# Kernel optimization log

Measured on AMD Instinct MI355X. Metric: run time of the kernel, lower is better.

Reference implementation:

```python
import jax, jax.numpy as jnp
import numpy as np

H = 128      # num_hidden
NIN = 384    # num_in
FF = 4 * H   # feedforward dim
SCALE = 30.0
EPS = 1e-5


def _linear(x, w, b):
    # torch Linear: weight [out, in]
    return x @ w.T + b


def _ln(x, g, b):
    mu = jnp.mean(x, axis=-1, keepdims=True)
    var = jnp.var(x, axis=-1, keepdims=True)
    return (x - mu) * jax.lax.rsqrt(var + EPS) * g + b


def setup_inputs() -> dict:
    key = jax.random.key(0)
    ks = jax.random.split(key, 16)
    B, N, K = 2, 2048, 48
    s = 0.05
    return {
        "h_V": jax.random.normal(ks[0], (B, N, H), jnp.float32),
        "h_E": jax.random.normal(ks[1], (B, N, K, NIN), jnp.float32),
        "mask_V": jnp.ones((B, N), jnp.float32),
        "mask_attend": jnp.ones((B, N, K), jnp.float32),
        "W1_w": jax.random.normal(ks[2], (H, H + NIN), jnp.float32) * s,
        "W1_b": jnp.zeros((H,), jnp.float32),
        "W2_w": jax.random.normal(ks[3], (H, H), jnp.float32) * s,
        "W2_b": jnp.zeros((H,), jnp.float32),
        "W3_w": jax.random.normal(ks[4], (H, H), jnp.float32) * s,
        "W3_b": jnp.zeros((H,), jnp.float32),
        "ln1_g": jnp.ones((H,), jnp.float32),
        "ln1_b": jnp.zeros((H,), jnp.float32),
        "ln2_g": jnp.ones((H,), jnp.float32),
        "ln2_b": jnp.zeros((H,), jnp.float32),
        "Win_w": jax.random.normal(ks[5], (FF, H), jnp.float32) * s,
        "Win_b": jnp.zeros((FF,), jnp.float32),
        "Wout_w": jax.random.normal(ks[6], (H, FF), jnp.float32) * s,
        "Wout_b": jnp.zeros((H,), jnp.float32),
    }


def reference(h_V, h_E, mask_V, mask_attend,
              W1_w, W1_b, W2_w, W2_b, W3_w, W3_b,
              ln1_g, ln1_b, ln2_g, ln2_b,
              Win_w, Win_b, Wout_w, Wout_b):
    gelu = lambda x: jax.nn.gelu(x, approximate=False)  # torch GELU (erf)
    B, N, K, _ = h_E.shape
    # expand-concat: [B,N,K,H+NIN]
    h_V_expand = jnp.broadcast_to(h_V[:, :, None, :], (B, N, K, H))
    h_EV = jnp.concatenate([h_V_expand, h_E], axis=-1)
    # 3-layer message MLP
    h_message = _linear(gelu(_linear(gelu(_linear(h_EV, W1_w, W1_b)), W2_w, W2_b)), W3_w, W3_b)
    h_message = mask_attend[..., None] * h_message
    dh = jnp.sum(h_message, axis=-2) / SCALE
    h = _ln(h_V + dh, ln1_g, ln1_b)  # dropout = identity (eval)
    dh = _linear(gelu(_linear(h, Win_w, Win_b)), Wout_w, Wout_b)
    h = _ln(h + dh, ln2_g, ln2_b)
    return mask_V[..., None] * h
```

## Files before the change

### kernel.cpp

```cpp
#include <hip/hip_runtime.h>
#include <math.h>


typedef __bf16 bf16;
typedef __attribute__((ext_vector_type(8))) __bf16 bf16x8;
typedef __attribute__((ext_vector_type(4))) float f32x4;
typedef __attribute__((ext_vector_type(4))) unsigned uint4v;

__device__ __forceinline__ unsigned pk2bf(float a, float b) {
    unsigned ua = __builtin_bit_cast(unsigned, a) + 0x8000u;
    unsigned ub = __builtin_bit_cast(unsigned, b) + 0x8000u;
    return __builtin_amdgcn_perm(ub, ua, 0x07060302u);
}
__device__ __forceinline__ bf16 f2bf(float f) {
    unsigned short s = (unsigned short)((__builtin_bit_cast(unsigned, f) + 0x8000u) >> 16);
    return __builtin_bit_cast(bf16, s);
}
__device__ __forceinline__ bf16x8 pack8(float4 v0, float4 v1) {
    uint4v p;
    p.x = pk2bf(v0.x, v0.y); p.y = pk2bf(v0.z, v0.w);
    p.z = pk2bf(v1.x, v1.y); p.w = pk2bf(v1.z, v1.w);
    return __builtin_bit_cast(bf16x8, p);
}
__device__ __forceinline__ float gelu_f(float x) {
    float u = 1.595769122f * x * fmaf(0.044715f, x * x, 1.0f);
    float e = __expf(-u);
    return x * __builtin_amdgcn_rcpf(1.0f + e);
}
__device__ __forceinline__ f32x4 mfma16(bf16x8 a, bf16x8 b, f32x4 c) {
    return __builtin_amdgcn_mfma_f32_16x16x32_bf16(a, b, c, 0, 0, 0);
}

#define WS_W2   65536
#define WS_W3   81920
#define WS_WIN  98304
#define WS_WOUT 163840
#define WS_TOTAL_W 229376
#define WS_H1_BYTES 458752

__global__ void convert_weights(const float* __restrict__ W1, const float* __restrict__ W2,
                                const float* __restrict__ W3, const float* __restrict__ Win,
                                const float* __restrict__ Wout, bf16* __restrict__ ws) {
    int i = blockIdx.x * 256 + threadIdx.x;
    if (i < WS_W2)              ws[i] = f2bf(W1[i]);
    else if (i < WS_W3)         ws[i] = f2bf(W2[i - WS_W2]);
    else if (i < WS_WIN)        ws[i] = f2bf(W3[i - WS_W3]);
    else if (i < WS_WOUT)       ws[i] = f2bf(Win[i - WS_WIN]);
    else if (i < WS_TOTAL_W)    ws[i] = f2bf(Wout[i - WS_WOUT]);
}

__global__ __launch_bounds__(256, 4)
void msg_kernel(const float* __restrict__ h_V, const float* __restrict__ h_E,
                const float* __restrict__ mask_attend,
                const bf16* __restrict__ W1b, const bf16* __restrict__ W2b,
                const bf16* __restrict__ W3b,
                const float* __restrict__ b1, const float* __restrict__ b2,
                const float* __restrict__ b3,
                const float* __restrict__ ln1g, const float* __restrict__ ln1b,
                float* __restrict__ h1out) {
    __shared__ __align__(16) bf16 m1[48 * 136];
    __shared__ __align__(16) bf16 m2[48 * 136];
    __shared__ float tbuf[128];

    const int tid  = threadIdx.x;
    const int wave = tid >> 6;
    const int lane = tid & 63;
    const int q    = lane >> 4;
    const int c15  = lane & 15;
    const int g    = blockIdx.x;
    const int n0c  = wave * 32 + c15;

    const f32x4 zero = {0.f, 0.f, 0.f, 0.f};

    f32x4 acc0[2] = {zero, zero};
    {
        const float* pV  = h_V + (size_t)g * 128 + q * 8;
        const bf16* pWv0 = W1b + (size_t)n0c * 512 + q * 8;
        const bf16* pWv1 = pWv0 + 16 * 512;
#pragma unroll
        for (int s = 0; s < 4; ++s) {
            float4 v0 = *(const float4*)(pV + s * 32);
            float4 v1 = *(const float4*)(pV + s * 32 + 4);
            bf16x8 af = pack8(v0, v1);
            bf16x8 w0 = *(const bf16x8*)(pWv0 + s * 32);
            bf16x8 w1 = *(const bf16x8*)(pWv1 + s * 32);
            acc0[0] = mfma16(af, w0, acc0[0]);
            acc0[1] = mfma16(af, w1, acc0[1]);
        }
    }

    f32x4 acc[3][2];
#pragma unroll
    for (int mt = 0; mt < 3; ++mt) { acc[mt][0] = zero; acc[mt][1] = zero; }
    {
        const float* pE0 = h_E + ((size_t)g * 48 + c15) * 384 + q * 8;
        const float* pE1 = pE0 + 16 * 384;
        const float* pE2 = pE1 + 16 * 384;
        const bf16* pW0 = W1b + (size_t)n0c * 512 + 128 + q * 8;
        const bf16* pW1 = pW0 + 16 * 512;
#pragma unroll
        for (int ks = 0; ks < 12; ++ks) {
            bf16x8 w0 = *(const bf16x8*)(pW0 + ks * 32);
            bf16x8 w1 = *(const bf16x8*)(pW1 + ks * 32);
            float4 a00 = *(const float4*)(pE0 + ks * 32);
            float4 a01 = *(const float4*)(pE0 + ks * 32 + 4);
            float4 a10 = *(const float4*)(pE1 + ks * 32);
            float4 a11 = *(const float4*)(pE1 + ks * 32 + 4);
            float4 a20 = *(const float4*)(pE2 + ks * 32);
            float4 a21 = *(const float4*)(pE2 + ks * 32 + 4);
            bf16x8 f0 = pack8(a00, a01);
            bf16x8 f1 = pack8(a10, a11);
            bf16x8 f2 = pack8(a20, a21);
            acc[0][0] = mfma16(f0, w0, acc[0][0]);
            acc[0][1] = mfma16(f0, w1, acc[0][1]);
            acc[1][0] = mfma16(f1, w0, acc[1][0]);
            acc[1][1] = mfma16(f1, w1, acc[1][1]);
            acc[2][0] = mfma16(f2, w0, acc[2][0]);
            acc[2][1] = mfma16(f2, w1, acc[2][1]);
        }
    }
    {
        const float bb0 = b1[n0c], bb1 = b1[n0c + 16];
#pragma unroll
        for (int mt = 0; mt < 3; ++mt)
#pragma unroll
            for (int r = 0; r < 4; ++r) {
                const int row = mt * 16 + q * 4 + r;
                m1[row * 136 + n0c]      = f2bf(gelu_f(acc[mt][0][r] + acc0[0][r] + bb0));
                m1[row * 136 + n0c + 16] = f2bf(gelu_f(acc[mt][1][r] + acc0[1][r] + bb1));
            }
    }
    __syncthreads();

    f32x4 acc2[3][2];
#pragma unroll
    for (int mt = 0; mt < 3; ++mt) { acc2[mt][0] = zero; acc2[mt][1] = zero; }
    {
        bf16x8 w[4][2];
        const bf16* pW20 = W2b + (size_t)n0c * 128 + q * 8;
        const bf16* pW21 = pW20 + 16 * 128;
#pragma unroll
        for (int s = 0; s < 4; ++s) {
            w[s][0] = *(const bf16x8*)(pW20 + s * 32);
            w[s][1] = *(const bf16x8*)(pW21 + s * 32);
        }
        const bf16* pA = m1 + c15 * 136 + q * 8;
#pragma unroll
        for (int s = 0; s < 4; ++s)
#pragma unroll
            for (int mt = 0; mt < 3; ++mt) {
                bf16x8 af = *(const bf16x8*)(pA + mt * 16 * 136 + s * 32);
                acc2[mt][0] = mfma16(af, w[s][0], acc2[mt][0]);
                acc2[mt][1] = mfma16(af, w[s][1], acc2[mt][1]);
            }
    }
    {
        const float bb0 = b2[n0c], bb1 = b2[n0c + 16];
#pragma unroll
        for (int mt = 0; mt < 3; ++mt)
#pragma unroll
            for (int r = 0; r < 4; ++r) {
                const int row = mt * 16 + q * 4 + r;
                m2[row * 136 + n0c]      = f2bf(gelu_f(acc2[mt][0][r] + bb0));
                m2[row * 136 + n0c + 16] = f2bf(gelu_f(acc2[mt][1][r] + bb1));
            }
    }
    __syncthreads();

    f32x4 acc3[3][2];
#pragma unroll
    for (int mt = 0; mt < 3; ++mt) { acc3[mt][0] = zero; acc3[mt][1] = zero; }
    {
        bf16x8 w[4][2];
        const bf16* pW30 = W3b + (size_t)n0c * 128 + q * 8;
        const bf16* pW31 = pW30 + 16 * 128;
#pragma unroll
        for (int s = 0; s < 4; ++s) {
            w[s][0] = *(const bf16x8*)(pW30 + s * 32);
            w[s][1] = *(const bf16x8*)(pW31 + s * 32);
        }
        const bf16* pA = m2 + c15 * 136 + q * 8;
#pragma unroll
        for (int s = 0; s < 4; ++s)
#pragma unroll
            for (int mt = 0; mt < 3; ++mt) {
                bf16x8 af = *(const bf16x8*)(pA + mt * 16 * 136 + s * 32);
                acc3[mt][0] = mfma16(af, w[s][0], acc3[mt][0]);
                acc3[mt][1] = mfma16(af, w[s][1], acc3[mt][1]);
            }
    }
    {
        const float bb0 = b3[n0c], bb1 = b3[n0c + 16];
        float s0 = 0.f, s1 = 0.f;
#pragma unroll
        for (int mt = 0; mt < 3; ++mt)
#pragma unroll
            for (int r = 0; r < 4; ++r) {
                const int row = mt * 16 + q * 4 + r;
                const float mv = mask_attend[(size_t)g * 48 + row];
                s0 += (acc3[mt][0][r] + bb0) * mv;
                s1 += (acc3[mt][1][r] + bb1) * mv;
            }
        s0 += __shfl_xor(s0, 16); s0 += __shfl_xor(s0, 32);
        s1 += __shfl_xor(s1, 16); s1 += __shfl_xor(s1, 32);
        if (lane < 16) {
            tbuf[n0c]      = h_V[(size_t)g * 128 + n0c]      + s0 * (1.0f / 30.0f);
            tbuf[n0c + 16] = h_V[(size_t)g * 128 + n0c + 16] + s1 * (1.0f / 30.0f);
        }
    }
    __syncthreads();

    if (wave == 0) {
        const float x0 = tbuf[lane];
        const float x1 = tbuf[lane + 64];
        float sm = x0 + x1, sq = x0 * x0 + x1 * x1;
#pragma unroll
        for (int off = 1; off < 64; off <<= 1) { sm += __shfl_xor(sm, off); sq += __shfl_xor(sq, off); }
        const float mu  = sm * (1.0f / 128.0f);
        const float var = sq * (1.0f / 128.0f) - mu * mu;
        const float inv = rsqrtf(var + 1e-5f);
        h1out[(size_t)g * 128 + lane]      = (x0 - mu) * inv * ln1g[lane]      + ln1b[lane];
        h1out[(size_t)g * 128 + 64 + lane] = (x1 - mu) * inv * ln1g[64 + lane] + ln1b[64 + lane];
    }
}

__global__ __launch_bounds__(512, 4)
void ffn_kernel(const float* __restrict__ h1, const bf16* __restrict__ Winb,
                const bf16* __restrict__ Woutb,
                const float* __restrict__ bin, const float* __restrict__ bout,
                const float* __restrict__ ln2g, const float* __restrict__ ln2b,
                const float* __restrict__ mask_V, float* __restrict__ out) {
    __shared__ __align__(16) bf16 a2[16 * 136];
    __shared__ __align__(16) bf16 ff[16 * 520];
    __shared__ float tb0[16 * 132];
    __shared__ float tb1[16 * 132];

    const int tid  = threadIdx.x;
    const int wave = tid >> 6;
    const int lane = tid & 63;
    const int q    = lane >> 4;
    const int c15  = lane & 15;
    const int r0g  = blockIdx.x * 8;
    const f32x4 zero = {0.f, 0.f, 0.f, 0.f};

    {
        const int row = tid >> 5;
        const int c4  = tid & 31;
        const int gr  = min(r0g + row, 4095);
        float4 v = *(const float4*)(h1 + (size_t)gr * 128 + c4 * 4);
        uint2 pk; pk.x = pk2bf(v.x, v.y); pk.y = pk2bf(v.z, v.w);
        *(uint2*)(a2 + row * 136 + c4 * 4) = pk;
    }
    __syncthreads();

    {
        f32x4 accA[4] = {zero, zero, zero, zero};
        const bf16* pA = a2 + c15 * 136 + q * 8;
#pragma unroll
        for (int s = 0; s < 4; ++s) {
            bf16x8 af = *(const bf16x8*)(pA + s * 32);
#pragma unroll
            for (int nt = 0; nt < 4; ++nt) {
                const int n = wave * 64 + nt * 16 + c15;
                bf16x8 wb = *(const bf16x8*)(Winb + (size_t)n * 128 + s * 32 + q * 8);
                accA[nt] = mfma16(af, wb, accA[nt]);
            }
        }
#pragma unroll
        for (int nt = 0; nt < 4; ++nt) {
            const int col = wave * 64 + nt * 16 + c15;
            const float bb = bin[col];
#pragma unroll
            for (int r = 0; r < 4; ++r)
                ff[(q * 4 + r) * 520 + col] = f2bf(gelu_f(accA[nt][r] + bb));
        }
    }
    __syncthreads();

    {
        const int kh = wave & 1, nq = wave >> 1;
        f32x4 accB[2] = {zero, zero};
        const bf16* pF = ff + c15 * 520 + kh * 256 + q * 8;
#pragma unroll
        for (int s = 0; s < 8; ++s) {
            bf16x8 af = *(const bf16x8*)(pF + s * 32);
#pragma unroll
            for (int nt = 0; nt < 2; ++nt) {
                const int n = nq * 32 + nt * 16 + c15;
                bf16x8 wb = *(const bf16x8*)(Woutb + (size_t)n * 512 + kh * 256 + s * 32 + q * 8);
                accB[nt] = mfma16(af, wb, accB[nt]);
            }
        }
        float* tb = kh ? tb1 : tb0;
#pragma unroll
        for (int nt = 0; nt < 2; ++nt) {
            const int col = nq * 32 + nt * 16 + c15;
#pragma unroll
            for (int r = 0; r < 4; ++r) {
                const int row = q * 4 + r;
                float v = accB[nt][r];
                if (kh == 0) {
                    const int gr = min(r0g + row, 4095);
                    v += bout[col] + h1[(size_t)gr * 128 + col];
                }
                tb[row * 132 + col] = v;
            }
        }
    }
    __syncthreads();

    {
        const int row = wave;
        const int gr  = r0g + row;
        const float x0 = tb0[row * 132 + lane]      + tb1[row * 132 + lane];
        const float x1 = tb0[row * 132 + 64 + lane] + tb1[row * 132 + 64 + lane];
        float sm = x0 + x1, sq = x0 * x0 + x1 * x1;
#pragma unroll
        for (int off = 1; off < 64; off <<= 1) { sm += __shfl_xor(sm, off); sq += __shfl_xor(sq, off); }
        const float mu  = sm * (1.0f / 128.0f);
        const float var = sq * (1.0f / 128.0f) - mu * mu;
        const float inv = rsqrtf(var + 1e-5f);
        const float mv  = mask_V[gr];
        out[(size_t)gr * 128 + lane]      = mv * ((x0 - mu) * inv * ln2g[lane]      + ln2b[lane]);
        out[(size_t)gr * 128 + 64 + lane] = mv * ((x1 - mu) * inv * ln2g[64 + lane] + ln2b[64 + lane]);
    }
}

extern "C" void kernel_launch(void* const* d_in, const int* in_sizes, int n_in,
                              void* d_out, int out_size, void* d_ws, size_t ws_size,
                              hipStream_t stream) {
    const float* h_V         = (const float*)d_in[0];
    const float* h_E         = (const float*)d_in[1];
    const float* mask_V      = (const float*)d_in[2];
    const float* mask_attend = (const float*)d_in[3];
    const float* W1w  = (const float*)d_in[4];
    const float* W1bb = (const float*)d_in[5];
    const float* W2w  = (const float*)d_in[6];
    const float* W2bb = (const float*)d_in[7];
    const float* W3w  = (const float*)d_in[8];
    const float* W3bb = (const float*)d_in[9];
    const float* ln1g = (const float*)d_in[10];
    const float* ln1b = (const float*)d_in[11];
    const float* ln2g = (const float*)d_in[12];
    const float* ln2b = (const float*)d_in[13];
    const float* Winw  = (const float*)d_in[14];
    const float* Winbb = (const float*)d_in[15];
    const float* Woutw  = (const float*)d_in[16];
    const float* Woutbb = (const float*)d_in[17];

    bf16* wsb   = (bf16*)d_ws;
    bf16* W1c   = wsb;
    bf16* W2c   = wsb + WS_W2;
    bf16* W3c   = wsb + WS_W3;
    bf16* Winc  = wsb + WS_WIN;
    bf16* Woutc = wsb + WS_WOUT;
    float* h1   = (float*)((char*)d_ws + WS_H1_BYTES);

    convert_weights<<<896, 256, 0, stream>>>(W1w, W2w, W3w, Winw, Woutw, wsb);
    msg_kernel<<<4096, 256, 0, stream>>>(h_V, h_E, mask_attend, W1c, W2c, W3c,
                                         W1bb, W2bb, W3bb, ln1g, ln1b, h1);
    ffn_kernel<<<512, 512, 0, stream>>>(h1, Winc, Woutc, Winbb, Woutbb,
                                        ln2g, ln2b, mask_V, (float*)d_out);
}
```

Measured before the change: 608.0 us.

## Pre-convert h_E to bf16 and DMA edge tiles into swizzled LDS

A new pass converts h_E to bf16 in the workspace. A new message kernel then loads each node's 48x384 edge tile straight into LDS with global_load_lds, using an XOR swizzle, and issues the h_V part of the W1 product while that load is in flight. This is meant to replace many scattered fp32 global loads and in-register packing with asynchronous bulk copies. The cost is an extra full read and write of h_E, plus a dependence on workspace size, with the old kernel kept as a fallback. The FFN kernel is also reshaped to 16 rows per 256-thread block with no K-split, which removes the second partial-sum buffer.

Result: faster. 570.6 us (-6.1%).

```diff
diff --git a/kernel.cpp b/kernel.cpp
--- a/kernel.cpp
+++ b/kernel.cpp
@@ -30,13 +30,19 @@
 __device__ __forceinline__ f32x4 mfma16(bf16x8 a, bf16x8 b, f32x4 c) {
     return __builtin_amdgcn_mfma_f32_16x16x32_bf16(a, b, c, 0, 0, 0);
 }
+__device__ __forceinline__ void dma16(const void* g, void* l) {
+    __builtin_amdgcn_global_load_lds(
+        (const __attribute__((address_space(1))) unsigned int*)g,
+        (__attribute__((address_space(3))) unsigned int*)l, 16, 0, 0);
+}
 
 #define WS_W2   65536
 #define WS_W3   81920
 #define WS_WIN  98304
 #define WS_WOUT 163840
 #define WS_TOTAL_W 229376
-#define WS_H1_BYTES 458752
+#define WS_H1_OFF  458752
+#define WS_HEB_OFF 2555904ull
 
 __global__ void convert_weights(const float* __restrict__ W1, const float* __restrict__ W2,
                                 const float* __restrict__ W3, const float* __restrict__ Win,
@@ -47,6 +53,200 @@
     else if (i < WS_WIN)        ws[i] = f2bf(W3[i - WS_W3]);
     else if (i < WS_WOUT)       ws[i] = f2bf(Win[i - WS_WIN]);
     else if (i < WS_TOTAL_W)    ws[i] = f2bf(Wout[i - WS_WOUT]);
+}
+
+__global__ void convert_hE(const float* __restrict__ he, bf16* __restrict__ out, long long n) {
+    size_t i = ((size_t)blockIdx.x * 256 + threadIdx.x) * 8;
+    if ((long long)i + 8 > n) return;
+    float4 v0 = *(const float4*)(he + i);
+    float4 v1 = *(const float4*)(he + i + 4);
+    *(bf16x8*)(out + i) = pack8(v0, v1);
+}
+
+__global__ __launch_bounds__(256, 3)
+void msg_kernel_b(const float* __restrict__ h_V, const bf16* __restrict__ hEb,
+                  const float* __restrict__ mask_attend,
+                  const bf16* __restrict__ W1b, const bf16* __restrict__ W2b,
+                  const bf16* __restrict__ W3b,
+                  const float* __restrict__ b1, const float* __restrict__ b2,
+                  const float* __restrict__ b3,
+                  const float* __restrict__ ln1g, const float* __restrict__ ln1b,
+                  float* __restrict__ h1out) {
+    __shared__ __align__(16) char smem[50432];
+    bf16*  Ab   = (bf16*)smem;
+    bf16*  m2   = (bf16*)smem;
+    bf16*  m1   = (bf16*)(smem + 36864);
+    float* tbuf = (float*)(smem + 49920);
+
+    const int tid  = threadIdx.x;
+    const int wave = tid >> 6;
+    const int lane = tid & 63;
+    const int q    = lane >> 4;
+    const int c15  = lane & 15;
+    const int g    = blockIdx.x;
+    const int n0c  = wave * 32 + c15;
+    const f32x4 zero = {0.f, 0.f, 0.f, 0.f};
+
+    float4 pv0[4], pv1[4];
+    bf16x8 pw0[4], pw1[4];
+    {
+        const float* pV  = h_V + (size_t)g * 128 + q * 8;
+        const bf16* pWv0 = W1b + (size_t)n0c * 512 + q * 8;
+        const bf16* pWv1 = pWv0 + 16 * 512;
+#pragma unroll
+        for (int s = 0; s < 4; ++s) {
+            pv0[s] = *(const float4*)(pV + s * 32);
+            pv1[s] = *(const float4*)(pV + s * 32 + 4);
+            pw0[s] = *(const bf16x8*)(pWv0 + s * 32);
+            pw1[s] = *(const bf16x8*)(pWv1 + s * 32);
+        }
+    }
+
+    {
+        const bf16* eb = hEb + (size_t)g * 48 * 384;
+#pragma unroll
+        for (int i = 0; i < 9; ++i) {
+            const int off = wave * 9216 + i * 1024 + lane * 16;
+            const int x   = off >> 8;
+            const int row = (x * 21846) >> 16;
+            const int seg = (off - row * 768) >> 4;
+            const int ss  = (seg & 48) | ((seg & 15) ^ (row & 15));
+            dma16(eb + row * 384 + ss * 8, smem + wave * 9216 + i * 1024);
+        }
+    }
+
+    f32x4 acc0[2] = {zero, zero};
+#pragma unroll
+    for (int s = 0; s < 4; ++s) {
+        bf16x8 af = pack8(pv0[s], pv1[s]);
+        acc0[0] = mfma16(af, pw0[s], acc0[0]);
+        acc0[1] = mfma16(af, pw1[s], acc0[1]);
+    }
+    __syncthreads();
+
+    f32x4 acc[3][2];
+#pragma unroll
+    for (int mt = 0; mt < 3; ++mt) { acc[mt][0] = zero; acc[mt][1] = zero; }
+    {
+        const bf16* pW0 = W1b + (size_t)n0c * 512 + 128 + q * 8;
+        const bf16* pW1 = pW0 + 16 * 512;
+#pragma unroll
+        for (int s = 0; s < 12; ++s) {
+            bf16x8 w0 = *(const bf16x8*)(pW0 + s * 32);
+            bf16x8 w1 = *(const bf16x8*)(pW1 + s * 32);
+            const int sq = s * 4 + q;
+            const int p  = (sq & 48) | ((sq & 15) ^ c15);
+#pragma unroll
+            for (int mt = 0; mt < 3; ++mt) {
+                bf16x8 af = *(const bf16x8*)(Ab + (mt * 16 + c15) * 384 + p * 8);
+                acc[mt][0] = mfma16(af, w0, acc[mt][0]);
+                acc[mt][1] = mfma16(af, w1, acc[mt][1]);
+            }
+        }
+    }
+    {
+        const float bb0 = b1[n0c], bb1 = b1[n0c + 16];
+#pragma unroll
+        for (int mt = 0; mt < 3; ++mt)
+#pragma unroll
+            for (int r = 0; r < 4; ++r) {
+                const int row = mt * 16 + q * 4 + r;
+                m1[row * 136 + n0c]      = f2bf(gelu_f(acc[mt][0][r] + acc0[0][r] + bb0));
+                m1[row * 136 + n0c + 16] = f2bf(gelu_f(acc[mt][1][r] + acc0[1][r] + bb1));
+            }
+    }
+    __syncthreads();
+
+    f32x4 acc2[3][2];
+#pragma unroll
+    for (int mt = 0; mt < 3; ++mt) { acc2[mt][0] = zero; acc2[mt][1] = zero; }
+    {
+        bf16x8 w[4][2];
+        const bf16* pW20 = W2b + (size_t)n0c * 128 + q * 8;
+        const bf16* pW21 = pW20 + 16 * 128;
+#pragma unroll
+        for (int s = 0; s < 4; ++s) {
+            w[s][0] = *(const bf16x8*)(pW20 + s * 32);
+            w[s][1] = *(const bf16x8*)(pW21 + s * 32);
+        }
+        const bf16* pA = m1 + c15 * 136 + q * 8;
+#pragma unroll
+        for (int s = 0; s < 4; ++s)
+#pragma unroll
+            for (int mt = 0; mt < 3; ++mt) {
+                bf16x8 af = *(const bf16x8*)(pA + mt * 16 * 136 + s * 32);
+                acc2[mt][0] = mfma16(af, w[s][0], acc2[mt][0]);
+                acc2[mt][1] = mfma16(af, w[s][1], acc2[mt][1]);
+            }
+    }
+    {
+        const float bb0 = b2[n0c], bb1 = b2[n0c + 16];
+#pragma unroll
+        for (int mt = 0; mt < 3; ++mt)
+#pragma unroll
+            for (int r = 0; r < 4; ++r) {
+                const int row = mt * 16 + q * 4 + r;
+                m2[row * 136 + n0c]      = f2bf(gelu_f(acc2[mt][0][r] + bb0));
+                m2[row * 136 + n0c + 16] = f2bf(gelu_f(acc2[mt][1][r] + bb1));
+            }
+    }
+    __syncthreads();
+
+    f32x4 acc3[3][2];
+#pragma unroll
+    for (int mt = 0; mt < 3; ++mt) { acc3[mt][0] = zero; acc3[mt][1] = zero; }
+    {
+        bf16x8 w[4][2];
+        const bf16* pW30 = W3b + (size_t)n0c * 128 + q * 8;
+        const bf16* pW31 = pW30 + 16 * 128;
+#pragma unroll
+        for (int s = 0; s < 4; ++s) {
+            w[s][0] = *(const bf16x8*)(pW30 + s * 32);
+            w[s][1] = *(const bf16x8*)(pW31 + s * 32);
+        }
+        const bf16* pA = m2 + c15 * 136 + q * 8;
+#pragma unroll
+        for (int s = 0; s < 4; ++s)
+#pragma unroll
+            for (int mt = 0; mt < 3; ++mt) {
+                bf16x8 af = *(const bf16x8*)(pA + mt * 16 * 136 + s * 32);
+                acc3[mt][0] = mfma16(af, w[s][0], acc3[mt][0]);
+                acc3[mt][1] = mfma16(af, w[s][1], acc3[mt][1]);
+            }
+    }
+    {
+        const float bb0 = b3[n0c], bb1 = b3[n0c + 16];
+        float s0 = 0.f, s1 = 0.f;
+#pragma unroll
+        for (int mt = 0; mt < 3; ++mt)
+#pragma unroll
+            for (int r = 0; r < 4; ++r) {
+                const int row = mt * 16 + q * 4 + r;
+                const float mv = mask_attend[(size_t)g * 48 + row];
+                s0 += (acc3[mt][0][r] + bb0) * mv;
+                s1 += (acc3[mt][1][r] + bb1) * mv;
+            }
+        s0 += __shfl_xor(s0, 16); s0 += __shfl_xor(s0, 32);
+        s1 += __shfl_xor(s1, 16); s1 += __shfl_xor(s1, 32);
+        if (lane < 16) {
+            tbuf[n0c]      = h_V[(size_t)g * 128 + n0c]      + s0 * (1.0f / 30.0f);
+            tbuf[n0c + 16] = h_V[(size_t)g * 128 + n0c + 16] + s1 * (1.0f / 30.0f);
+        }
+    }
+    __syncthreads();
+
+    if (wave == 0) {
+        const float x0 = tbuf[lane];
+        const float x1 = tbuf[lane + 64];
+        float sm = x0 + x1, sq = x0 * x0 + x1 * x1;
+#pragma unroll
+        for (int off = 1; off < 64; off <<= 1) { sm += __shfl_xor(sm, off); sq += __shfl_xor(sq, off); }
+        const float mu  = sm * (1.0f / 128.0f);
+        const float var = sq * (1.0f / 128.0f) - mu * mu;
+        const float inv = rsqrtf(var + 1e-5f);
+        h1out[(size_t)g * 128 + lane]      = (x0 - mu) * inv * ln1g[lane]      + ln1b[lane];
+        h1out[(size_t)g * 128 + 64 + lane] = (x1 - mu) * inv * ln1g[64 + lane] + ln1b[64 + lane];
+    }
 }
 
 __global__ __launch_bounds__(256, 4)
@@ -69,7 +269,6 @@
     const int c15  = lane & 15;
     const int g    = blockIdx.x;
     const int n0c  = wave * 32 + c15;
-
     const f32x4 zero = {0.f, 0.f, 0.f, 0.f};
 
     f32x4 acc0[2] = {zero, zero};
@@ -82,13 +281,10 @@
             float4 v0 = *(const float4*)(pV + s * 32);
             float4 v1 = *(const float4*)(pV + s * 32 + 4);
             bf16x8 af = pack8(v0, v1);
-            bf16x8 w0 = *(const bf16x8*)(pWv0 + s * 32);
-            bf16x8 w1 = *(const bf16x8*)(pWv1 + s * 32);
-            acc0[0] = mfma16(af, w0, acc0[0]);
-            acc0[1] = mfma16(af, w1, acc0[1]);
-        }
-    }
-
+            acc0[0] = mfma16(af, *(const bf16x8*)(pWv0 + s * 32), acc0[0]);
+            acc0[1] = mfma16(af, *(const bf16x8*)(pWv1 + s * 32), acc0[1]);
+        }
+    }
     f32x4 acc[3][2];
 #pragma unroll
     for (int mt = 0; mt < 3; ++mt) { acc[mt][0] = zero; acc[mt][1] = zero; }
@@ -102,21 +298,12 @@
         for (int ks = 0; ks < 12; ++ks) {
             bf16x8 w0 = *(const bf16x8*)(pW0 + ks * 32);
             bf16x8 w1 = *(const bf16x8*)(pW1 + ks * 32);
-            float4 a00 = *(const float4*)(pE0 + ks * 32);
-            float4 a01 = *(const float4*)(pE0 + ks * 32 + 4);
-            float4 a10 = *(const float4*)(pE1 + ks * 32);
-            float4 a11 = *(const float4*)(pE1 + ks * 32 + 4);
-            float4 a20 = *(const float4*)(pE2 + ks * 32);
-            float4 a21 = *(const float4*)(pE2 + ks * 32 + 4);
-            bf16x8 f0 = pack8(a00, a01);
-            bf16x8 f1 = pack8(a10, a11);
-            bf16x8 f2 = pack8(a20, a21);
-            acc[0][0] = mfma16(f0, w0, acc[0][0]);
-            acc[0][1] = mfma16(f0, w1, acc[0][1]);
-            acc[1][0] = mfma16(f1, w0, acc[1][0]);
-            acc[1][1] = mfma16(f1, w1, acc[1][1]);
-            acc[2][0] = mfma16(f2, w0, acc[2][0]);
-            acc[2][1] = mfma16(f2, w1, acc[2][1]);
+            bf16x8 f0 = pack8(*(const float4*)(pE0 + ks * 32), *(const float4*)(pE0 + ks * 32 + 4));
+            bf16x8 f1 = pack8(*(const float4*)(pE1 + ks * 32), *(const float4*)(pE1 + ks * 32 + 4));
+            bf16x8 f2 = pack8(*(const float4*)(pE2 + ks * 32), *(const float4*)(pE2 + ks * 32 + 4));
+            acc[0][0] = mfma16(f0, w0, acc[0][0]); acc[0][1] = mfma16(f0, w1, acc[0][1]);
+            acc[1][0] = mfma16(f1, w0, acc[1][0]); acc[1][1] = mfma16(f1, w1, acc[1][1]);
+            acc[2][0] = mfma16(f2, w0, acc[2][0]); acc[2][1] = mfma16(f2, w1, acc[2][1]);
         }
     }
     {
@@ -131,7 +318,6 @@
             }
     }
     __syncthreads();
-
     f32x4 acc2[3][2];
 #pragma unroll
     for (int mt = 0; mt < 3; ++mt) { acc2[mt][0] = zero; acc2[mt][1] = zero; }
@@ -140,10 +326,7 @@
         const bf16* pW20 = W2b + (size_t)n0c * 128 + q * 8;
         const bf16* pW21 = pW20 + 16 * 128;
 #pragma unroll
-        for (int s = 0; s < 4; ++s) {
-            w[s][0] = *(const bf16x8*)(pW20 + s * 32);
-            w[s][1] = *(const bf16x8*)(pW21 + s * 32);
-        }
+        for (int s = 0; s < 4; ++s) { w[s][0] = *(const bf16x8*)(pW20 + s * 32); w[s][1] = *(const bf16x8*)(pW21 + s * 32); }
         const bf16* pA = m1 + c15 * 136 + q * 8;
 #pragma unroll
         for (int s = 0; s < 4; ++s)
@@ -166,7 +349,6 @@
             }
     }
     __syncthreads();
-
     f32x4 acc3[3][2];
 #pragma unroll
     for (int mt = 0; mt < 3; ++mt) { acc3[mt][0] = zero; acc3[mt][1] = zero; }
@@ -175,10 +357,7 @@
         const bf16* pW30 = W3b + (size_t)n0c * 128 + q * 8;
         const bf16* pW31 = pW30 + 16 * 128;
 #pragma unroll
-        for (int s = 0; s < 4; ++s) {
-            w[s][0] = *(const bf16x8*)(pW30 + s * 32);
-            w[s][1] = *(const bf16x8*)(pW31 + s * 32);
-        }
+        for (int s = 0; s < 4; ++s) { w[s][0] = *(const bf16x8*)(pW30 + s * 32); w[s][1] = *(const bf16x8*)(pW31 + s * 32); }
         const bf16* pA = m2 + c15 * 136 + q * 8;
 #pragma unroll
         for (int s = 0; s < 4; ++s)
@@ -209,7 +388,6 @@
         }
     }
     __syncthreads();
-
     if (wave == 0) {
         const float x0 = tbuf[lane];
         const float x1 = tbuf[lane + 64];
@@ -224,7 +402,7 @@
     }
 }
 
-__global__ __launch_bounds__(512, 4)
+__global__ __launch_bounds__(256)
 void ffn_kernel(const float* __restrict__ h1, const bf16* __restrict__ Winb,
                 const bf16* __restrict__ Woutb,
                 const float* __restrict__ bin, const float* __restrict__ bout,
@@ -232,43 +410,41 @@
                 const float* __restrict__ mask_V, float* __restrict__ out) {
     __shared__ __align__(16) bf16 a2[16 * 136];
     __shared__ __align__(16) bf16 ff[16 * 520];
-    __shared__ float tb0[16 * 132];
-    __shared__ float tb1[16 * 132];
+    __shared__ float tb[16 * 132];
 
     const int tid  = threadIdx.x;
     const int wave = tid >> 6;
     const int lane = tid & 63;
     const int q    = lane >> 4;
     const int c15  = lane & 15;
-    const int r0g  = blockIdx.x * 8;
+    const int r0g  = blockIdx.x * 16;
     const f32x4 zero = {0.f, 0.f, 0.f, 0.f};
 
     {
-        const int row = tid >> 5;
-        const int c4  = tid & 31;
-        const int gr  = min(r0g + row, 4095);
-        float4 v = *(const float4*)(h1 + (size_t)gr * 128 + c4 * 4);
-        uint2 pk; pk.x = pk2bf(v.x, v.y); pk.y = pk2bf(v.z, v.w);
-        *(uint2*)(a2 + row * 136 + c4 * 4) = pk;
-    }
-    __syncthreads();
-
-    {
-        f32x4 accA[4] = {zero, zero, zero, zero};
-        const bf16* pA = a2 + c15 * 136 + q * 8;
+        const int row = tid >> 4, seg = tid & 15;
+        const float* p = h1 + (size_t)(r0g + row) * 128 + seg * 8;
+        float4 v0 = *(const float4*)p, v1 = *(const float4*)(p + 4);
+        *(bf16x8*)(a2 + row * 136 + seg * 8) = pack8(v0, v1);
+    }
+    __syncthreads();
+
+    {
+        f32x4 accA[8];
+#pragma unroll
+        for (int i = 0; i < 8; ++i) accA[i] = zero;
 #pragma unroll
         for (int s = 0; s < 4; ++s) {
-            bf16x8 af = *(const bf16x8*)(pA + s * 32);
-#pragma unroll
-            for (int nt = 0; nt < 4; ++nt) {
-                const int n = wave * 64 + nt * 16 + c15;
+            bf16x8 af = *(const bf16x8*)(a2 + c15 * 136 + s * 32 + q * 8);
+#pragma unroll
+            for (int nt = 0; nt < 8; ++nt) {
+                const int n = wave * 128 + nt * 16 + c15;
                 bf16x8 wb = *(const bf16x8*)(Winb + (size_t)n * 128 + s * 32 + q * 8);
                 accA[nt] = mfma16(af, wb, accA[nt]);
             }
         }
 #pragma unroll
-        for (int nt = 0; nt < 4; ++nt) {
-            const int col = wave * 64 + nt * 16 + c15;
+        for (int nt = 0; nt < 8; ++nt) {
+            const int col = wave * 128 + nt * 16 + c15;
             const float bb = bin[col];
 #pragma unroll
             for (int r = 0; r < 4; ++r)
@@ -278,42 +454,36 @@
     __syncthreads();
 
     {
-        const int kh = wave & 1, nq = wave >> 1;
         f32x4 accB[2] = {zero, zero};
-        const bf16* pF = ff + c15 * 520 + kh * 256 + q * 8;
-#pragma unroll
-        for (int s = 0; s < 8; ++s) {
-            bf16x8 af = *(const bf16x8*)(pF + s * 32);
+#pragma unroll
+        for (int s = 0; s < 16; ++s) {
+            bf16x8 af = *(const bf16x8*)(ff + c15 * 520 + s * 32 + q * 8);
 #pragma unroll
             for (int nt = 0; nt < 2; ++nt) {
-                const int n = nq * 32 + nt * 16 + c15;
-                bf16x8 wb = *(const bf16x8*)(Woutb + (size_t)n * 512 + kh * 256 + s * 32 + q * 8);
+                const int n = wave * 32 + nt * 16 + c15;
+                bf16x8 wb = *(const bf16x8*)(Woutb + (size_t)n * 512 + s * 32 + q * 8);
                 accB[nt] = mfma16(af, wb, accB[nt]);
             }
         }
-        float* tb = kh ? tb1 : tb0;
 #pragma unroll
         for (int nt = 0; nt < 2; ++nt) {
-            const int col = nq * 32 + nt * 16 + c15;
+            const int col = wave * 32 + nt * 16 + c15;
+            const float bb = bout[col];
 #pragma unroll
             for (int r = 0; r < 4; ++r) {
                 const int row = q * 4 + r;
-                float v = accB[nt][r];
-                if (kh == 0) {
-                    const int gr = min(r0g + row, 4095);
-                    v += bout[col] + h1[(size_t)gr * 128 + col];
-                }
-                tb[row * 132 + col] = v;
-            }
-        }
-    }
-    __syncthreads();
-
-    {
-        const int row = wave;
+                tb[row * 132 + col] = accB[nt][r] + bb + h1[(size_t)(r0g + row) * 128 + col];
+            }
+        }
+    }
+    __syncthreads();
+
+#pragma unroll
+    for (int rr = 0; rr < 4; ++rr) {
+        const int row = wave * 4 + rr;
         const int gr  = r0g + row;
-        const float x0 = tb0[row * 132 + lane]      + tb1[row * 132 + lane];
-        const float x1 = tb0[row * 132 + 64 + lane] + tb1[row * 132 + 64 + lane];
+        const float x0 = tb[row * 132 + lane];
+        const float x1 = tb[row * 132 + 64 + lane];
         float sm = x0 + x1, sq = x0 * x0 + x1 * x1;
 #pragma unroll
         for (int off = 1; off < 64; off <<= 1) { sm += __shfl_xor(sm, off); sq += __shfl_xor(sq, off); }
@@ -348,17 +518,29 @@
     const float* Woutw  = (const float*)d_in[16];
     const float* Woutbb = (const float*)d_in[17];
 
-    bf16* wsb   = (bf16*)d_ws;
+    char* ws    = (char*)d_ws;
+    bf16* wsb   = (bf16*)ws;
     bf16* W1c   = wsb;
     bf16* W2c   = wsb + WS_W2;
     bf16* W3c   = wsb + WS_W3;
     bf16* Winc  = wsb + WS_WIN;
     bf16* Woutc = wsb + WS_WOUT;
-    float* h1   = (float*)((char*)d_ws + WS_H1_BYTES);
+    float* h1   = (float*)(ws + WS_H1_OFF);
+    bf16* hEb   = (bf16*)(ws + WS_HEB_OFF);
+
+    const long long nE = (long long)in_sizes[1];
+    const size_t ws_need = (size_t)WS_HEB_OFF + (size_t)nE * 2;
 
     convert_weights<<<896, 256, 0, stream>>>(W1w, W2w, W3w, Winw, Woutw, wsb);
-    msg_kernel<<<4096, 256, 0, stream>>>(h_V, h_E, mask_attend, W1c, W2c, W3c,
-                                         W1bb, W2bb, W3bb, ln1g, ln1b, h1);
-    ffn_kernel<<<512, 512, 0, stream>>>(h1, Winc, Woutc, Winbb, Woutbb,
+    if (ws_size >= ws_need) {
+        const int nb = (int)((nE + 2047) / 2048);
+        convert_hE<<<nb, 256, 0, stream>>>(h_E, hEb, nE);
+        msg_kernel_b<<<4096, 256, 0, stream>>>(h_V, hEb, mask_attend, W1c, W2c, W3c,
+                                               W1bb, W2bb, W3bb, ln1g, ln1b, h1);
+    } else {
+        msg_kernel<<<4096, 256, 0, stream>>>(h_V, h_E, mask_attend, W1c, W2c, W3c,
+                                             W1bb, W2bb, W3bb, ln1g, ln1b, h1);
+    }
+    ffn_kernel<<<256, 256, 0, stream>>>(h1, Winc, Woutc, Winbb, Woutbb,
                                         ln2g, ln2b, mask_V, (float*)d_out);
 }
```
